# Kernel tuning notes

Hardware: AMD Instinct MI355X
Metric: run time of the kernel (lower is better)

## Reference

```python
import jax, jax.numpy as jnp
import numpy as np

V, D, T, B = 50257, 1024, 512, 4
H = 4 * D  # mlp hidden for encoder/decoder stand-ins


def setup_inputs() -> dict:
    key = jax.random.key(0)
    ks = jax.random.split(key, 16)
    sc = 0.02
    n = lambda k, shape: (jax.random.normal(k, shape, jnp.float32) * sc)
    return {
        'input_ids': jax.random.randint(ks[0], (B, 1, T), 0, V),
        'labels': jax.random.randint(ks[1], (B, T), 0, V),
        'wte': n(ks[2], (V, D)),
        'enc_w1': n(ks[3], (D, H)), 'enc_b1': jnp.zeros((H,), jnp.float32),
        'enc_w2': n(ks[4], (H, D)), 'enc_b2': jnp.zeros((D,), jnp.float32),
        'proj_w': n(ks[5], (D // 2, D)), 'proj_b': jnp.zeros((D,), jnp.float32),
        'dec_w1': n(ks[6], (D, H)), 'dec_b1': jnp.zeros((H,), jnp.float32),
        'dec_w2': n(ks[7], (H, D)), 'dec_b2': jnp.zeros((D,), jnp.float32),
        'lm_w': n(ks[8], (D, V)),
    }


def reference(input_ids, labels, wte, enc_w1, enc_b1, enc_w2, enc_b2,
              proj_w, proj_b, dec_w1, dec_b1, dec_w2, dec_b2, lm_w):
    dim = wte.shape[1]
    half = dim // 2
    tlen = input_ids.shape[-1]
    x = jnp.squeeze(input_ids, 1)                     # [B, T]
    h = wte[x]                                        # [B, T, D] embedding
    # encoder (token-wise MLP stand-in)
    h = jax.nn.gelu(h @ enc_w1 + enc_b1) @ enc_w2 + enc_b2
    e = h[:, -1, :]                                   # [B, D] last-token embedding
    # sliding overlapping windows: window i = e[i : i+dim//2] (single vectorized gather)
    idx = (jnp.arange(tlen)[:, None] + jnp.arange(half)[None, :]) % dim  # [T, D/2]
    windows = e[:, idx]                               # [B, T, D/2]
    p = windows @ proj_w + proj_b                     # [B, T, D]
    # decoder (token-wise MLP stand-in)
    d = jax.nn.gelu(p @ dec_w1 + dec_b1) @ dec_w2 + dec_b2
    logits = jnp.einsum('btd,dv->btv', d, lm_w)       # [B, T, V]
    output = jnp.transpose(logits, (0, 2, 1))         # [B, V, T] as in rearrange
    logp = jax.nn.log_softmax(output, axis=1)
    nll = -jnp.take_along_axis(logp, labels[:, None, :], axis=1)  # [B, 1, T]
    loss = jnp.mean(nll)
    return (loss, output)
```

## Files before the change

kernel.cpp:

```cpp
#include <hip/hip_runtime.h>

#define VSZ 50257
#define DSZ 1024
#define TSZ 512
#define BSZ 4
#define HSZ 4096
#define VPAD 50432
#define NCH (VPAD / 64)
#define NPOS 2048
#define QS 16.0f
#define DQS (1.0f / 256.0f)
#define CG 64
#define CPC 13

typedef __attribute__((ext_vector_type(4))) float f32x4;
typedef __attribute__((ext_vector_type(16))) float f32x16;
typedef __attribute__((ext_vector_type(4))) int i32x4;
typedef __attribute__((ext_vector_type(8))) int i32x8;

#define GLD16(gp, lp) __builtin_amdgcn_global_load_lds( \
  (const __attribute__((address_space(1))) unsigned int*)(gp), \
  (__attribute__((address_space(3))) unsigned int*)(lp), 16, 0, 0)

__device__ __forceinline__ float gelu_f(float x) {
  float x3 = x * x * x;
  float u = 0.7978845608028654f * (x + 0.044715f * x3);
  return 0.5f * x * (1.f + tanhf(u));
}

__device__ __forceinline__ unsigned char q8(float v) {
  return (unsigned char)__builtin_amdgcn_cvt_pk_fp8_f32(v * QS, v * QS, 0, 0);
}

#define KS1 8
#define KS2 16
__global__ __launch_bounds__(256) void transpose_all(
    const float* __restrict__ lm_w, const float* __restrict__ dw1,
    const float* __restrict__ dw2, const float* __restrict__ pw,
    unsigned char* __restrict__ lm8, unsigned char* __restrict__ w18,
    unsigned char* __restrict__ w28, unsigned char* __restrict__ p8,
    const int* __restrict__ ids, const float* __restrict__ wte,
    const float* __restrict__ w1, float* __restrict__ t1p) {
  __shared__ float tile[64][65];
  int bid = blockIdx.x;
  int tid = threadIdx.x;

  if (bid >= 14784) {
    int eb = bid - 14784;
    int h = (eb & 15) * 256 + tid;
    int kc = eb >> 4;
    float (*ev)[128] = (float(*)[128])tile;
    for (int i = tid; i < 512; i += 256) {
      int b = i >> 7, d = i & 127;
      int tok = ids[b * TSZ + (TSZ - 1)];
      ev[b][d] = wte[(size_t)tok * DSZ + kc * 128 + d];
    }
    __syncthreads();
    const float* w = w1 + (size_t)(kc * 128) * HSZ + h;
    float s0 = 0.f, s1 = 0.f, s2 = 0.f, s3 = 0.f;
#pragma unroll 4
    for (int d = 0; d < 128; ++d) {
      float wv = w[(size_t)d * HSZ];
      s0 += ev[0][d] * wv; s1 += ev[1][d] * wv;
      s2 += ev[2][d] * wv; s3 += ev[3][d] * wv;
    }
    t1p[((size_t)(0 * KS1 + kc)) * HSZ + h] = s0;
    t1p[((size_t)(1 * KS1 + kc)) * HSZ + h] = s1;
    t1p[((size_t)(2 * KS1 + kc)) * HSZ + h] = s2;
    t1p[((size_t)(3 * KS1 + kc)) * HSZ + h] = s3;
    return;
  }

  const float* src; unsigned char* dst; int R, C, Cpad, bx, by;
  if (bid < 12608)      { src = lm_w; dst = lm8; R = DSZ; C = VSZ; Cpad = VPAD; bx = bid % 788; by = bid / 788; }
  else if (bid < 13632) { int b = bid - 12608; src = dw1; dst = w18; R = DSZ; C = HSZ; Cpad = HSZ; bx = b % 64; by = b / 64; }
  else if (bid < 14656) { int b = bid - 13632; src = dw2; dst = w28; R = HSZ; C = DSZ; Cpad = DSZ; bx = b % 16; by = b / 16; }
  else                  { int b = bid - 14656; src = pw;  dst = p8;  R = 512; C = DSZ; Cpad = DSZ; bx = b % 16; by = b / 16; }
  int c0 = bx * 64, r0 = by * 64;
  int wv = tid >> 6, ln = tid & 63;
  int c = c0 + ln;
#pragma unroll 4
  for (int i = 0; i < 16; ++i) {
    int r = i * 4 + wv;
    tile[r][ln] = (c < C) ? src[(size_t)(r0 + r) * C + c] : 0.f;
  }
  __syncthreads();
  int ccb = tid >> 4;
  int r4 = (tid & 15) * 4;
#pragma unroll
  for (int j = 0; j < 4; ++j) {
    int cc = ccb + j * 16;
    if (c0 + cc >= Cpad) continue;
    unsigned int u = __builtin_amdgcn_cvt_pk_fp8_f32(QS * tile[r4 + 0][cc], QS * tile[r4 + 1][cc], 0, 0);
    u = __builtin_amdgcn_cvt_pk_fp8_f32(QS * tile[r4 + 2][cc], QS * tile[r4 + 3][cc], u, 1);
    *(unsigned int*)(dst + (size_t)(c0 + cc) * R + r0 + r4) = u;
  }
}

__global__ __launch_bounds__(256) void enc2p_kernel(const float* __restrict__ t1p,
                                                    const float* __restrict__ b1,
                                                    const float* __restrict__ w2,
                                                    float* __restrict__ ep) {
  __shared__ float ts[4][256];
  int i = blockIdx.x * 256 + threadIdx.x;
  int kc = blockIdx.y;
  int h = kc * 256 + threadIdx.x;
  float bv = b1[h];
#pragma unroll
  for (int b = 0; b < 4; ++b) {
    float s0 = bv;
#pragma unroll
    for (int cc = 0; cc < KS1; ++cc) s0 += t1p[((size_t)(b * KS1 + cc)) * HSZ + h];
    ts[b][threadIdx.x] = gelu_f(s0);
  }
  __syncthreads();
  const float* w = w2 + (size_t)(kc * 256) * DSZ + i;
  float a0 = 0.f, a1 = 0.f, a2 = 0.f, a3 = 0.f;
#pragma unroll 4
  for (int j = 0; j < 256; ++j) {
    float wv = w[(size_t)j * DSZ];
    a0 += ts[0][j] * wv; a1 += ts[1][j] * wv;
    a2 += ts[2][j] * wv; a3 += ts[3][j] * wv;
  }
  ep[((size_t)(0 * KS2 + kc)) * DSZ + i] = a0;
  ep[((size_t)(1 * KS2 + kc)) * DSZ + i] = a1;
  ep[((size_t)(2 * KS2 + kc)) * DSZ + i] = a2;
  ep[((size_t)(3 * KS2 + kc)) * DSZ + i] = a3;
}

__global__ __launch_bounds__(256) void win8_kernel(const float* __restrict__ ep,
                                                   const float* __restrict__ b2,
                                                   unsigned char* __restrict__ win8) {
  int blk = blockIdx.x;
  int b = blk >> 9, t = blk & 511;
  const float* epb = ep + (size_t)b * KS2 * DSZ;
  for (int j = threadIdx.x; j < 512; j += 256) {
    int d = t + j;
    float s = b2[d];
#pragma unroll
    for (int kc = 0; kc < KS2; ++kc) s += epb[(size_t)kc * DSZ + d];
    win8[(size_t)blk * 512 + j] = q8(s);
  }
}

template<int GELU>
__global__ __launch_bounds__(256, 3) void gemmMX0(
    const unsigned char* __restrict__ A, const unsigned char* __restrict__ Bm,
    const float* __restrict__ bias, unsigned char* __restrict__ out8,
    int NT, int N, int K) {
  __shared__ __align__(16) char SM[49152];
  const int tid = threadIdx.x;
  const int lane = tid & 63;
  const int wave = tid >> 6;
  const int wr = (wave >> 1) * 64, wc = (wave & 1) * 64;
  const int l31 = lane & 31, hi = lane >> 5;

  const int cpx = (int)gridDim.x >> 3;
  const int wg = ((int)blockIdx.x & 7) * cpx + ((int)blockIdx.x >> 3);
  const int m0 = (wg / NT) * 128, n0 = (wg % NT) * 128;

  f32x16 acc[2][2];
#pragma unroll
  for (int i = 0; i < 2; ++i)
#pragma unroll
    for (int j = 0; j < 2; ++j)
#pragma unroll
      for (int r = 0; r < 16; ++r) acc[i][j][r] = 0.f;

  const int ppair = lane & 3;
  const int row0 = wave * 16 + (lane >> 2);
  const int row1 = row0 + 64;
  const int og0 = (ppair - (row0 >> 1)) & 3;
  const int og1 = (ppair - (row1 >> 1)) & 3;
  const unsigned char* a0 = A + (size_t)(m0 + row0) * K + og0 * 16;
  const unsigned char* a1 = A + (size_t)(m0 + row1) * K + og1 * 16;
  const unsigned char* b0 = Bm + (size_t)(n0 + row0) * K + og0 * 16;
  const unsigned char* b1 = Bm + (size_t)(n0 + row1) * K + og1 * 16;

#define STGM(tt, bufb) do { \
    GLD16(a0 + (size_t)(tt) * 64, SM + (bufb) + wave * 1024); \
    GLD16(a1 + (size_t)(tt) * 64, SM + (bufb) + 4096 + wave * 1024); \
    GLD16(b0 + (size_t)(tt) * 64, SM + (bufb) + 8192 + wave * 1024); \
    GLD16(b1 + (size_t)(tt) * 64, SM + (bufb) + 12288 + wave * 1024); \
  } while (0)

  const int KT = K >> 6;
  STGM(0, 0);
  STGM(1, 16384);
  asm volatile("s_waitcnt vmcnt(4)" ::: "memory");
  __builtin_amdgcn_s_barrier();
  asm volatile("" ::: "memory");
  int cb = 0;
  for (int t = 0; t < KT; ++t) {
    if (t + 2 < KT) {
      int nb = cb + 32768; if (nb >= 49152) nb -= 49152;
      STGM(t + 2, nb);
    }
    i32x8 a8[2], b8[2];
#pragma unroll
    for (int mf = 0; mf < 2; ++mf) {
      const int row = wr + mf * 32 + l31;
      const char* base = SM + cb + row * 64;
      const int ph0 = (2 * hi + (row >> 1)) & 3;
      const int ph1 = (2 * hi + 1 + (row >> 1)) & 3;
      i32x4 q01 = *(const i32x4*)(base + ph0 * 16);
      i32x4 q23 = *(const i32x4*)(base + ph1 * 16);
      a8[mf] = __builtin_shufflevector(q01, q23, 0, 1, 2, 3, 4, 5, 6, 7);
    }
#pragma unroll
    for (int nf = 0; nf < 2; ++nf) {
      const int row = wc + nf * 32 + l31;
      const char* base = SM + cb + 8192 + row * 64;
      const int ph0 = (2 * hi + (row >> 1)) & 3;
      const int ph1 = (2 * hi + 1 + (row >> 1)) & 3;
      i32x4 q01 = *(const i32x4*)(base + ph0 * 16);
      i32x4 q23 = *(const i32x4*)(base + ph1 * 16);
      b8[nf] = __builtin_shufflevector(q01, q23, 0, 1, 2, 3, 4, 5, 6, 7);
    }
#pragma unroll
    for (int mf = 0; mf < 2; ++mf)
#pragma unroll
      for (int nf = 0; nf < 2; ++nf)
        acc[mf][nf] = __builtin_amdgcn_mfma_scale_f32_32x32x64_f8f6f4(
            a8[mf], b8[nf], acc[mf][nf], 0, 0, 0, 123, 0, 123);
    if (t + 2 < KT) {
      asm volatile("s_waitcnt vmcnt(4) lgkmcnt(0)" ::: "memory");
      __builtin_amdgcn_s_barrier();
      asm volatile("" ::: "memory");
    } else if (t + 1 < KT) {
      asm volatile("s_waitcnt vmcnt(0) lgkmcnt(0)" ::: "memory");
      __builtin_amdgcn_s_barrier();
      asm volatile("" ::: "memory");
    }
    cb += 16384; if (cb >= 49152) cb = 0;
  }
#undef STGM
  asm volatile("s_waitcnt lgkmcnt(0)" ::: "memory");

#pragma unroll
  for (int nf = 0; nf < 2; ++nf) {
    const int n = n0 + wc + nf * 32 + l31;
    const float bv = bias[n];
#pragma unroll
    for (int mf = 0; mf < 2; ++mf) {
      const int mb = m0 + wr + mf * 32 + 4 * hi;
#pragma unroll
      for (int r = 0; r < 16; ++r) {
        const int m = mb + (r & 3) + 8 * (r >> 2);
        float v = acc[mf][nf][r] + bv;
        if (GELU) v = gelu_f(v);
        out8[(size_t)m * N + n] = q8(v);
      }
    }
  }
}

__global__ __launch_bounds__(256, 3) void gemmLM(
    const unsigned char* __restrict__ A, const unsigned char* __restrict__ Bm,
    float* __restrict__ outF, float* __restrict__ pm, float* __restrict__ ps) {
  __shared__ __align__(16) char SM[49152];
  const int tid = threadIdx.x;
  const int lane = tid & 63;
  const int wave = tid >> 6;
  const int wr = (wave >> 1) * 64, wc = (wave & 1) * 64;
  const int l31 = lane & 31, hi = lane >> 5;

  const int cpx = (int)gridDim.x >> 3;
  const int wg = ((int)blockIdx.x & 7) * cpx + ((int)blockIdx.x >> 3);
  const int m0 = (wg >> 4) * 128, n0 = (wg & 15) * 128;

  f32x16 acc[2][2];
#pragma unroll
  for (int i = 0; i < 2; ++i)
#pragma unroll
    for (int j = 0; j < 2; ++j)
#pragma unroll
      for (int r = 0; r < 16; ++r) acc[i][j][r] = 0.f;

  const int ppair = lane & 3;
  const int row0 = wave * 16 + (lane >> 2);
  const int row1 = row0 + 64;
  const int og0 = (ppair - (row0 >> 1)) & 3;
  const int og1 = (ppair - (row1 >> 1)) & 3;
  const unsigned char* a0 = A + (size_t)(m0 + row0) * DSZ + og0 * 16;
  const unsigned char* a1 = A + (size_t)(m0 + row1) * DSZ + og1 * 16;
  const unsigned char* b0 = Bm + (size_t)(n0 + row0) * DSZ + og0 * 16;
  const unsigned char* b1 = Bm + (size_t)(n0 + row1) * DSZ + og1 * 16;

#define STGL(tt, bufb) do { \
    GLD16(a0 + (size_t)(tt) * 64, SM + (bufb) + wave * 1024); \
    GLD16(a1 + (size_t)(tt) * 64, SM + (bufb) + 4096 + wave * 1024); \
    GLD16(b0 + (size_t)(tt) * 64, SM + (bufb) + 8192 + wave * 1024); \
    GLD16(b1 + (size_t)(tt) * 64, SM + (bufb) + 12288 + wave * 1024); \
  } while (0)

  STGL(0, 0);
  STGL(1, 16384);
  asm volatile("s_waitcnt vmcnt(4)" ::: "memory");
  __builtin_amdgcn_s_barrier();
  asm volatile("" ::: "memory");
  int cb = 0;
  for (int t = 0; t < 16; ++t) {
    if (t + 2 < 16) {
      int nb = cb + 32768; if (nb >= 49152) nb -= 49152;
      STGL(t + 2, nb);
    }
    i32x8 a8[2], b8[2];
#pragma unroll
    for (int mf = 0; mf < 2; ++mf) {
      const int row = wr + mf * 32 + l31;
      const char* base = SM + cb + row * 64;
      const int ph0 = (2 * hi + (row >> 1)) & 3;
      const int ph1 = (2 * hi + 1 + (row >> 1)) & 3;
      i32x4 q01 = *(const i32x4*)(base + ph0 * 16);
      i32x4 q23 = *(const i32x4*)(base + ph1 * 16);
      a8[mf] = __builtin_shufflevector(q01, q23, 0, 1, 2, 3, 4, 5, 6, 7);
    }
#pragma unroll
    for (int nf = 0; nf < 2; ++nf) {
      const int row = wc + nf * 32 + l31;
      const char* base = SM + cb + 8192 + row * 64;
      const int ph0 = (2 * hi + (row >> 1)) & 3;
      const int ph1 = (2 * hi + 1 + (row >> 1)) & 3;
      i32x4 q01 = *(const i32x4*)(base + ph0 * 16);
      i32x4 q23 = *(const i32x4*)(base + ph1 * 16);
      b8[nf] = __builtin_shufflevector(q01, q23, 0, 1, 2, 3, 4, 5, 6, 7);
    }
#pragma unroll
    for (int mf = 0; mf < 2; ++mf)
#pragma unroll
      for (int nf = 0; nf < 2; ++nf)
        acc[mf][nf] = __builtin_amdgcn_mfma_scale_f32_32x32x64_f8f6f4(
            a8[mf], b8[nf], acc[mf][nf], 0, 0, 0, 123, 0, 123);
    if (t + 2 < 16) {
      asm volatile("s_waitcnt vmcnt(4) lgkmcnt(0)" ::: "memory");
      __builtin_amdgcn_s_barrier();
      asm volatile("" ::: "memory");
    } else if (t + 1 < 16) {
      asm volatile("s_waitcnt vmcnt(0) lgkmcnt(0)" ::: "memory");
      __builtin_amdgcn_s_barrier();
      asm volatile("" ::: "memory");
    }
    cb += 16384; if (cb >= 49152) cb = 0;
  }
#undef STGL
  asm volatile("s_waitcnt lgkmcnt(0)" ::: "memory");

  const int ch = (m0 + wr) >> 6;
#pragma unroll
  for (int nf = 0; nf < 2; ++nf) {
    const int pos = n0 + wc + nf * 32 + l31;
    float mloc = -1e30f, sloc = 0.f;
#pragma unroll
    for (int mf = 0; mf < 2; ++mf) {
      const int vb = m0 + wr + mf * 32 + 4 * hi;
#pragma unroll
      for (int r = 0; r < 16; ++r) {
        const int v = vb + (r & 3) + 8 * (r >> 2);
        if (v < VSZ) mloc = fmaxf(mloc, acc[mf][nf][r]);
      }
    }
#pragma unroll
    for (int mf = 0; mf < 2; ++mf) {
      const int vb = m0 + wr + mf * 32 + 4 * hi;
#pragma unroll
      for (int r = 0; r < 16; ++r) {
        const int v = vb + (r & 3) + 8 * (r >> 2);
        if (v < VSZ) sloc += __expf(acc[mf][nf][r] - mloc);
      }
    }
    {
      float mo = __shfl_xor(mloc, 32, 64);
      float so = __shfl_xor(sloc, 32, 64);
      float nm = fmaxf(mloc, mo);
      sloc = sloc * __expf(mloc - nm) + so * __expf(mo - nm);
      mloc = nm;
    }
    if (hi == 0) {
      pm[(size_t)ch * NPOS + pos] = mloc;
      ps[(size_t)ch * NPOS + pos] = sloc;
    }
  }

  float* epi = (float*)SM;
  const int bb = n0 >> 9, t0 = n0 & 511;
  float* outG = outF + 1 + (size_t)bb * VSZ * TSZ + t0;
  const int trow = tid >> 5;
  const int lofs = (tid & 31) * 4;
#pragma unroll
  for (int p = 0; p < 2; ++p) {
    __builtin_amdgcn_s_barrier();
    asm volatile("" ::: "memory");
    {
      const int rg = wave >> 1;
#pragma unroll
      for (int nf = 0; nf < 2; ++nf)
#pragma unroll
        for (int r = 0; r < 16; ++r)
          epi[rg * 4224 + ((r & 3) + 8 * (r >> 2) + 4 * hi) * 132 + wc + nf * 32 + l31] =
              acc[p][nf][r];
    }
    __builtin_amdgcn_s_barrier();
    asm volatile("" ::: "memory");
#pragma unroll
    for (int rg = 0; rg < 2; ++rg) {
      const int q = rg * 2 + p;
#pragma unroll
      for (int pp = 0; pp < 4; ++pp) {
        int row = pp * 8 + trow;
        int v = m0 + q * 32 + row;
        if (v < VSZ) {
          f32x4 val = *(const f32x4*)&epi[rg * 4224 + row * 132 + lofs];
          float* gp = outG + (size_t)v * TSZ + lofs;
          __builtin_nontemporal_store(val[0], gp + 0);
          __builtin_nontemporal_store(val[1], gp + 1);
          __builtin_nontemporal_store(val[2], gp + 2);
          __builtin_nontemporal_store(val[3], gp + 3);
        }
      }
    }
  }
}

__global__ __launch_bounds__(256) void lsestage1_kernel(const float* __restrict__ pm,
                                                        const float* __restrict__ ps,
                                                        float* __restrict__ pm2,
                                                        float* __restrict__ ps2) {
  int pos = (blockIdx.x & 7) * 256 + threadIdx.x;
  int cg = blockIdx.x >> 3;
  int c0 = cg * CPC;
  int c1 = c0 + CPC; if (c1 > NCH) c1 = NCH;
  float m = -1e30f, s = 0.f;
  for (int c = c0; c < c1; ++c) {
    float cm = pm[(size_t)c * NPOS + pos];
    float cs = ps[(size_t)c * NPOS + pos];
    float nm = fmaxf(m, cm);
    s = s * __expf(m - nm) + cs * __expf(cm - nm);
    m = nm;
  }
  pm2[(size_t)cg * NPOS + pos] = m;
  ps2[(size_t)cg * NPOS + pos] = s;
}

__global__ __launch_bounds__(256) void lsemerge_kernel(const float* __restrict__ pm2,
                                                       const float* __restrict__ ps2,
                                                       const float* __restrict__ outF,
                                                       const int* __restrict__ labels,
                                                       float* __restrict__ contrib) {
  int pos = blockIdx.x * 256 + threadIdx.x;
  float m[4] = {-1e30f, -1e30f, -1e30f, -1e30f};
  float s[4] = {0.f, 0.f, 0.f, 0.f};
  for (int c = 0; c < CG; c += 4) {
#pragma unroll
    for (int j = 0; j < 4; ++j) {
      float cm = pm2[(size_t)(c + j) * NPOS + pos];
      float cs = ps2[(size_t)(c + j) * NPOS + pos];
      float nm = fmaxf(m[j], cm);
      s[j] = s[j] * __expf(m[j] - nm) + cs * __expf(cm - nm);
      m[j] = nm;
    }
  }
#pragma unroll
  for (int j = 1; j < 4; ++j) {
    float nm = fmaxf(m[0], m[j]);
    s[0] = s[0] * __expf(m[0] - nm) + s[j] * __expf(m[j] - nm);
    m[0] = nm;
  }
  float lse = m[0] + logf(s[0]);
  int b = pos >> 9, t = pos & 511;
  int lab = labels[pos];
  float x = outF[1 + (size_t)b * VSZ * TSZ + (size_t)lab * TSZ + t];
  contrib[pos] = lse - x;
}

__global__ __launch_bounds__(256) void lossfinal_kernel(const float* __restrict__ contrib,
                                                        float* __restrict__ dout) {
  __shared__ float red[256];
  int tid = threadIdx.x;
  float a = 0.f;
  for (int i = tid; i < NPOS; i += 256) a += contrib[i];
  red[tid] = a;
  __syncthreads();
  for (int off = 128; off; off >>= 1) {
    if (tid < off) red[tid] += red[tid + off];
    __syncthreads();
  }
  if (tid == 0) dout[0] = red[0] / (float)NPOS;
}

extern "C" void kernel_launch(void* const* d_in, const int* in_sizes, int n_in,
                              void* d_out, int out_size, void* d_ws, size_t ws_size,
                              hipStream_t stream) {
  const int* input_ids = (const int*)d_in[0];
  const int* labels    = (const int*)d_in[1];
  const float* wte     = (const float*)d_in[2];
  const float* enc_w1  = (const float*)d_in[3];
  const float* enc_b1  = (const float*)d_in[4];
  const float* enc_w2  = (const float*)d_in[5];
  const float* enc_b2  = (const float*)d_in[6];
  const float* proj_w  = (const float*)d_in[7];
  const float* proj_b  = (const float*)d_in[8];
  const float* dec_w1  = (const float*)d_in[9];
  const float* dec_b1  = (const float*)d_in[10];
  const float* dec_w2  = (const float*)d_in[11];
  const float* dec_b2  = (const float*)d_in[12];
  const float* lm_w    = (const float*)d_in[13];
  float* outF = (float*)d_out;

  char* w = (char*)d_ws;
  size_t off = 0;
  unsigned char* lm8  = (unsigned char*)(w + off); off += (size_t)VPAD * DSZ;
  unsigned char* w18  = (unsigned char*)(w + off); off += (size_t)HSZ * DSZ;
  unsigned char* w28  = (unsigned char*)(w + off); off += (size_t)DSZ * HSZ;
  unsigned char* p8   = (unsigned char*)(w + off); off += (size_t)DSZ * 512;
  unsigned char* win8 = (unsigned char*)(w + off); off += (size_t)NPOS * 512;
  unsigned char* pbuf8= (unsigned char*)(w + off); off += (size_t)NPOS * DSZ;
  unsigned char* abuf8= (unsigned char*)(w + off); off += (size_t)NPOS * HSZ;
  unsigned char* dbuf8= (unsigned char*)(w + off); off += (size_t)NPOS * DSZ;
  float* t1p    = (float*)(w + off);  off += (size_t)BSZ * KS1 * HSZ * 4;
  float* ep     = (float*)(w + off);  off += (size_t)BSZ * KS2 * DSZ * 4;
  float* contrib= (float*)(w + off);  off += (size_t)NPOS * 4;
  float* pm     = (float*)(w + off);  off += (size_t)NCH * NPOS * 4;
  float* ps     = (float*)(w + off);  off += (size_t)NCH * NPOS * 4;
  float* pm2    = (float*)(w + off);  off += (size_t)CG * NPOS * 4;
  float* ps2    = (float*)(w + off);  off += (size_t)CG * NPOS * 4;
  (void)ws_size; (void)in_sizes; (void)n_in; (void)out_size;

  transpose_all<<<14912, 256, 0, stream>>>(lm_w, dec_w1, dec_w2, proj_w,
                                           lm8, w18, w28, p8,
                                           input_ids, wte, enc_w1, t1p);

  enc2p_kernel<<<dim3(DSZ / 256, KS2), 256, 0, stream>>>(t1p, enc_b1, enc_w2, ep);
  win8_kernel<<<2048, 256, 0, stream>>>(ep, enc_b2, win8);

  gemmMX0<0><<<128, 256, 0, stream>>>(win8, p8, proj_b, pbuf8, 8, DSZ, 512);
  gemmMX0<1><<<512, 256, 0, stream>>>(pbuf8, w18, dec_b1, abuf8, 32, HSZ, DSZ);
  gemmMX0<0><<<128, 256, 0, stream>>>(abuf8, w28, dec_b2, dbuf8, 8, DSZ, HSZ);
  gemmLM<<<6304, 256, 0, stream>>>(lm8, dbuf8, outF, pm, ps);

  lsestage1_kernel<<<512, 256, 0, stream>>>(pm, ps, pm2, ps2);
  lsemerge_kernel<<<dim3(NPOS / 256), 256, 0, stream>>>(pm2, ps2, outF, labels, contrib);
  lossfinal_kernel<<<1, 256, 0, stream>>>(contrib, outF);
}
```

Baseline: 364.4 us.

## Shrink LM GEMM LDS to double buffer for higher occupancy

Cuts gemmLM shared memory from a 48KB triple buffer to a 32KB double buffer and raises launch_bounds min-blocks from 3 to 5 so more workgroups fit per CU. The K-loop now prefetches only one tile ahead with a barrier before and after each compute step. The epilogue transpose staging is split into four 32-row passes so it fits the smaller buffer. The trade-off is a shallower prefetch, more barriers and a tighter register budget, which may spill.

```diff
diff --git a/kernel.cpp b/kernel.cpp
--- a/kernel.cpp
+++ b/kernel.cpp
@@ -255,10 +255,10 @@
   }
 }
 
-__global__ __launch_bounds__(256, 3) void gemmLM(
+__global__ __launch_bounds__(256, 5) void gemmLM(
     const unsigned char* __restrict__ A, const unsigned char* __restrict__ Bm,
     float* __restrict__ outF, float* __restrict__ pm, float* __restrict__ ps) {
-  __shared__ __align__(16) char SM[49152];
+  __shared__ __align__(16) char SM[32768];
   const int tid = threadIdx.x;
   const int lane = tid & 63;
   const int wave = tid >> 6;
@@ -295,16 +295,16 @@
   } while (0)
 
   STGL(0, 0);
-  STGL(1, 16384);
-  asm volatile("s_waitcnt vmcnt(4)" ::: "memory");
-  __builtin_amdgcn_s_barrier();
-  asm volatile("" ::: "memory");
-  int cb = 0;
   for (int t = 0; t < 16; ++t) {
-    if (t + 2 < 16) {
-      int nb = cb + 32768; if (nb >= 49152) nb -= 49152;
-      STGL(t + 2, nb);
-    }
+    const int cb = (t & 1) << 14;
+    if (t + 1 < 16) {
+      STGL(t + 1, cb ^ 16384);
+      asm volatile("s_waitcnt vmcnt(4)" ::: "memory");
+    } else {
+      asm volatile("s_waitcnt vmcnt(0)" ::: "memory");
+    }
+    __builtin_amdgcn_s_barrier();
+    asm volatile("" ::: "memory");
     i32x8 a8[2], b8[2];
 #pragma unroll
     for (int mf = 0; mf < 2; ++mf) {
@@ -332,19 +332,11 @@
       for (int nf = 0; nf < 2; ++nf)
         acc[mf][nf] = __builtin_amdgcn_mfma_scale_f32_32x32x64_f8f6f4(
             a8[mf], b8[nf], acc[mf][nf], 0, 0, 0, 123, 0, 123);
-    if (t + 2 < 16) {
-      asm volatile("s_waitcnt vmcnt(4) lgkmcnt(0)" ::: "memory");
-      __builtin_amdgcn_s_barrier();
-      asm volatile("" ::: "memory");
-    } else if (t + 1 < 16) {
-      asm volatile("s_waitcnt vmcnt(0) lgkmcnt(0)" ::: "memory");
-      __builtin_amdgcn_s_barrier();
-      asm volatile("" ::: "memory");
-    }
-    cb += 16384; if (cb >= 49152) cb = 0;
+    asm volatile("s_waitcnt lgkmcnt(0)" ::: "memory");
+    __builtin_amdgcn_s_barrier();
+    asm volatile("" ::: "memory");
   }
 #undef STGL
-  asm volatile("s_waitcnt lgkmcnt(0)" ::: "memory");
 
   const int ch = (m0 + wr) >> 6;
 #pragma unroll
@@ -388,35 +380,31 @@
   const int trow = tid >> 5;
   const int lofs = (tid & 31) * 4;
 #pragma unroll
-  for (int p = 0; p < 2; ++p) {
+  for (int q = 0; q < 4; ++q) {
     __builtin_amdgcn_s_barrier();
     asm volatile("" ::: "memory");
-    {
-      const int rg = wave >> 1;
+    if ((wave >> 1) == (q >> 1)) {
+      const int mf = q & 1;
 #pragma unroll
       for (int nf = 0; nf < 2; ++nf)
 #pragma unroll
         for (int r = 0; r < 16; ++r)
-          epi[rg * 4224 + ((r & 3) + 8 * (r >> 2) + 4 * hi) * 132 + wc + nf * 32 + l31] =
-              acc[p][nf][r];
+          epi[((r & 3) + 8 * (r >> 2) + 4 * hi) * 132 + wc + nf * 32 + l31] =
+              acc[mf][nf][r];
     }
     __builtin_amdgcn_s_barrier();
     asm volatile("" ::: "memory");
 #pragma unroll
-    for (int rg = 0; rg < 2; ++rg) {
-      const int q = rg * 2 + p;
-#pragma unroll
-      for (int pp = 0; pp < 4; ++pp) {
-        int row = pp * 8 + trow;
-        int v = m0 + q * 32 + row;
-        if (v < VSZ) {
-          f32x4 val = *(const f32x4*)&epi[rg * 4224 + row * 132 + lofs];
-          float* gp = outG + (size_t)v * TSZ + lofs;
-          __builtin_nontemporal_store(val[0], gp + 0);
-          __builtin_nontemporal_store(val[1], gp + 1);
-          __builtin_nontemporal_store(val[2], gp + 2);
-          __builtin_nontemporal_store(val[3], gp + 3);
-        }
+    for (int pp = 0; pp < 4; ++pp) {
+      int row = pp * 8 + trow;
+      int v = m0 + q * 32 + row;
+      if (v < VSZ) {
+        f32x4 val = *(const f32x4*)&epi[row * 132 + lofs];
+        float* gp = outG + (size_t)v * TSZ + lofs;
+        __builtin_nontemporal_store(val[0], gp + 0);
+        __builtin_nontemporal_store(val[1], gp + 1);
+        __builtin_nontemporal_store(val[2], gp + 2);
+        __builtin_nontemporal_store(val[3], gp + 3);
       }
     }
   }
```

After: 1.182 ms. 224% more time.
